# Kernel optimization log

Measured on AMD Instinct MI355X. Metric: run time of the kernel, lower is better.

Reference implementation:

```python
import jax, jax.numpy as jnp
import numpy as np

B, C, H, W = 4, 512, 56, 56
G, K = 16, 3
P = K * K
GC = C // G
DWK = 3
PAD = 1
OFFSET_SCALE = 1.0


def setup_inputs():
    key = jax.random.key(0)
    ks = jax.random.split(key, 10)

    def w(i, shape, sc=0.02):
        return jax.random.normal(ks[i], shape, jnp.float32) * sc

    return {
        "x": jax.random.normal(ks[0], (B, C, H, W), jnp.float32),
        "w_in": w(1, (C, C)), "b_in": jnp.zeros((C,), jnp.float32),
        "w_dw": w(2, (DWK, DWK, 1, C)), "b_dw": jnp.zeros((C,), jnp.float32),
        "ln_g": jnp.ones((C,), jnp.float32), "ln_b": jnp.zeros((C,), jnp.float32),
        "w_off": w(3, (C, G * P * 2)), "b_off": jnp.zeros((G * P * 2,), jnp.float32),
        "w_mask": w(4, (C, G * P)), "b_mask": jnp.zeros((G * P,), jnp.float32),
        "w_out": w(5, (C, C)), "b_out": jnp.zeros((C,), jnp.float32),
        "bn_g": jnp.ones((C,), jnp.float32), "bn_b": jnp.zeros((C,), jnp.float32),
        "bn_m": w(6, (C,), 0.1), "bn_v": jnp.abs(w(7, (C,), 0.1)) + 1.0,
    }


def _dcnv3_core(xp, offset, mask):
    """xp: [B,H,W,C]; offset: [B,H,W,G*P*2]; mask (softmaxed over P): [B,H,W,G,P]."""
    xpad = jnp.pad(xp, ((0, 0), (PAD, PAD), (PAD, PAD), (0, 0)))
    Hin, Win = H + 2 * PAD, W + 2 * PAD
    # normalized reference points (output-location centers in padded input coords)
    ref_x = (jnp.arange(W, dtype=jnp.float32) + 0.5 + (K - 1) // 2) / Win
    ref_y = (jnp.arange(H, dtype=jnp.float32) + 0.5 + (K - 1) // 2) / Hin
    # dilation grid, kx-major / ky-minor flattening (matches InternImage core)
    k = jnp.arange(K, dtype=jnp.float32) - (K - 1) // 2
    gx = jnp.repeat(k, K) / Win  # [P]
    gy = jnp.tile(k, K) / Hin    # [P]
    off = offset.reshape(B, H, W, G, P, 2)
    lx = ref_x[None, None, :, None, None] + gx * OFFSET_SCALE + off[..., 0] * OFFSET_SCALE / Win
    ly = ref_y[None, :, None, None, None] + gy * OFFSET_SCALE + off[..., 1] * OFFSET_SCALE / Hin
    # grid_sample semantics, align_corners=False, zero padding
    px = lx * Win - 0.5
    py = ly * Hin - 0.5
    x0f = jnp.floor(px)
    y0f = jnp.floor(py)
    tx = px - x0f
    ty = py - y0f
    x0 = x0f.astype(jnp.int32)
    y0 = y0f.astype(jnp.int32)
    flat = xpad.reshape(B, Hin * Win * G, GC)
    gidx = jnp.arange(G)[None, None, :, None]

    def corner(fb, yi, xi):
        valid = (yi >= 0) & (yi < Hin) & (xi >= 0) & (xi < Win)
        idx = (jnp.clip(yi, 0, Hin - 1) * Win + jnp.clip(xi, 0, Win - 1)) * G + gidx
        return jnp.take(fb, idx, axis=0) * valid[..., None]  # [H,W,G,P,GC]

    def sample_one(fb, y0b, x0b, tyb, txb):
        w00 = ((1 - tyb) * (1 - txb))[..., None]
        w01 = ((1 - tyb) * txb)[..., None]
        w10 = (tyb * (1 - txb))[..., None]
        w11 = (tyb * txb)[..., None]
        return (corner(fb, y0b, x0b) * w00 + corner(fb, y0b, x0b + 1) * w01
                + corner(fb, y0b + 1, x0b) * w10 + corner(fb, y0b + 1, x0b + 1) * w11)

    samp = jax.vmap(sample_one)(flat, y0, x0, ty, tx)  # [B,H,W,G,P,GC]
    return jnp.einsum('bhwgpc,bhwgp->bhwgc', samp, mask).reshape(B, H, W, C)


def reference(x, w_in, b_in, w_dw, b_dw, ln_g, ln_b, w_off, b_off, w_mask, b_mask, w_out, b_out, bn_g, bn_b, bn_m, bn_v):
    xh = jnp.transpose(x, (0, 2, 3, 1))  # NCHW -> NHWC
    xp = xh @ w_in + b_in                # input_proj
    # offset/mask branch: depthwise conv + LayerNorm(channels) + GELU
    x1 = jax.lax.conv_general_dilated(xh, w_dw, (1, 1), 'SAME', feature_group_count=C,
                                      dimension_numbers=('NHWC', 'HWIO', 'NHWC')) + b_dw
    mu = x1.mean(-1, keepdims=True)
    var = x1.var(-1, keepdims=True)
    x1 = (x1 - mu) / jnp.sqrt(var + 1e-6) * ln_g + ln_b
    x1 = jax.nn.gelu(x1, approximate=False)
    offset = x1 @ w_off + b_off
    mask = jax.nn.softmax((x1 @ w_mask + b_mask).reshape(B, H, W, G, P), axis=-1)
    y = _dcnv3_core(xp, offset, mask)
    y = y @ w_out + b_out                # output_proj
    y = jnp.transpose(y, (0, 3, 1, 2))   # NHWC -> NCHW
    # BatchNorm2d (inference: running stats) + SiLU
    y = (y - bn_m[:, None, None]) / jnp.sqrt(bn_v[:, None, None] + 1e-5) * bn_g[:, None, None] + bn_b[:, None, None]
    return jax.nn.silu(y)
```

## Files before the change

kernel.cpp:

```cpp
#include <hip/hip_runtime.h>
#include <cmath>

constexpr int B_ = 4, C_ = 512, H_ = 56, W_ = 56;
constexpr int HW_ = H_ * W_;
constexpr int NPIX = B_ * HW_;
constexpr int G_ = 16, P_ = 9;
constexpr int NMSK = G_ * P_;

typedef __attribute__((ext_vector_type(8))) short short8;
typedef __attribute__((ext_vector_type(4))) float f32x4;

__device__ __forceinline__ float b2f(ushort u) {
    union { unsigned int i; float f; } v; v.i = (unsigned int)u << 16; return v.f;
}
__device__ __forceinline__ ushort f2b(float f) {
    unsigned int x = __float_as_uint(f);
    unsigned int r = (x + 0x7fffu + ((x >> 16) & 1u)) >> 16;
    return (ushort)r;
}
__device__ __forceinline__ void gload16(const ushort* g, ushort* l) {
    __builtin_amdgcn_global_load_lds(
        (const __attribute__((address_space(1))) unsigned int*)g,
        (__attribute__((address_space(3))) unsigned int*)l, 16, 0, 0);
}

__global__ __launch_bounds__(256) void prep_weights_kernel(
    const float* __restrict__ w_in, const float* __restrict__ w_off,
    const float* __restrict__ w_mask, const float* __restrict__ w_out,
    const float* __restrict__ b_off, const float* __restrict__ b_mask,
    ushort* __restrict__ wtA, ushort* __restrict__ wtOM, ushort* __restrict__ wtO,
    float* __restrict__ bOM)
{
    __shared__ float tile[32][33];
    int z = blockIdx.z;
    int k0 = blockIdx.x * 32;
    int n0 = blockIdx.y * 32;
    int tx = threadIdx.x, ty = threadIdx.y;
    for (int i = ty; i < 32; i += 8) {
        int k = k0 + i, n = n0 + tx;
        float v;
        if (z == 0) v = w_in[k * 512 + n];
        else if (z == 1) v = w_out[k * 512 + n];
        else v = (n < 288) ? w_off[k * 288 + n]
                           : (n < 432 ? w_mask[k * 144 + (n - 288)] : 0.f);
        tile[i][tx] = v;
    }
    __syncthreads();
    ushort* dst = (z == 0) ? wtA : (z == 1 ? wtO : wtOM);
    for (int i = ty; i < 32; i += 8)
        dst[(size_t)(n0 + i) * 512 + k0 + tx] = f2b(tile[tx][i]);
    if (z == 2 && blockIdx.x == 0 && blockIdx.y == 0) {
        int t = ty * 32 + tx;
        for (int tt = t; tt < 512; tt += 256)
            bOM[tt] = (tt < 288) ? b_off[tt] : (tt < 432 ? b_mask[tt - 288] : 0.f);
    }
}

__global__ __launch_bounds__(256) void transpose_in_kernel(
    const float* __restrict__ in, ushort* __restrict__ out)
{
    __shared__ float tile[32][33];
    int b = blockIdx.z;
    int hw0 = blockIdx.x * 32;
    int c0 = blockIdx.y * 32;
    int tx = threadIdx.x, ty = threadIdx.y;
    const float* ib = in + (size_t)b * C_ * HW_;
    #pragma unroll
    for (int i = ty; i < 32; i += 8)
        tile[i][tx] = ib[(size_t)(c0 + i) * HW_ + hw0 + tx];
    __syncthreads();
    ushort* ob = out + (size_t)b * HW_ * C_;
    #pragma unroll
    for (int i = ty; i < 32; i += 8)
        ob[(size_t)(hw0 + i) * C_ + c0 + tx] = f2b(tile[tx][i]);
}

template <int MODE>
__global__ __launch_bounds__(256) void mfma_gemm_kernel(
    const ushort* __restrict__ A, const ushort* __restrict__ Bt,
    const float* __restrict__ bias, void* __restrict__ Cout,
    const float* __restrict__ bng, const float* __restrict__ bnb,
    const float* __restrict__ bnm, const float* __restrict__ bnv)
{
    __shared__ ushort As[128 * 64];
    __shared__ ushort Bs[128 * 64];
    int tid = threadIdx.x;
    int lane = tid & 63, wid = tid >> 6;
    int row0 = blockIdx.x * 128, col0 = blockIdx.y * 128;
    int wm = wid >> 1, wn = wid & 1;

    f32x4 acc[4][4] = {};

    int lr = lane >> 3;
    int sc = (lane & 7) ^ lr;

    for (int k0 = 0; k0 < 512; k0 += 64) {
        if (k0) __syncthreads();
        #pragma unroll
        for (int i = 0; i < 4; i++) {
            int rb = (wid * 4 + i) * 8;
            gload16(A + (size_t)(row0 + rb + lr) * 512 + k0 + sc * 8, &As[rb * 64]);
            gload16(Bt + (size_t)(col0 + rb + lr) * 512 + k0 + sc * 8, &Bs[rb * 64]);
        }
        __syncthreads();
        #pragma unroll
        for (int ks = 0; ks < 2; ks++) {
            short8 af[4], bf[4];
            #pragma unroll
            for (int mi = 0; mi < 4; mi++) {
                int r = wm * 64 + mi * 16 + (lane & 15);
                int c = ((lane >> 4) + ks * 4) ^ (r & 7);
                af[mi] = *(const short8*)((const char*)As + r * 128 + c * 16);
            }
            #pragma unroll
            for (int ni = 0; ni < 4; ni++) {
                int r = wn * 64 + ni * 16 + (lane & 15);
                int c = ((lane >> 4) + ks * 4) ^ (r & 7);
                bf[ni] = *(const short8*)((const char*)Bs + r * 128 + c * 16);
            }
            #pragma unroll
            for (int mi = 0; mi < 4; mi++)
                #pragma unroll
                for (int ni = 0; ni < 4; ni++)
                    acc[mi][ni] = __builtin_amdgcn_mfma_f32_16x16x32_bf16(
                        af[mi], bf[ni], acc[mi][ni], 0, 0, 0);
        }
    }

    #pragma unroll
    for (int ni = 0; ni < 4; ni++) {
        int col = col0 + wn * 64 + ni * 16 + (lane & 15);
        float bv = bias[col];
        float bsc = 0.f, bsh = 0.f;
        if constexpr (MODE == 2) {
            float inv = rsqrtf(bnv[col] + 1e-5f);
            bsc = bng[col] * inv;
            bsh = bnb[col] - bnm[col] * bsc;
        }
        #pragma unroll
        for (int mi = 0; mi < 4; mi++) {
            int rowb = row0 + wm * 64 + mi * 16 + (lane >> 4) * 4;
            #pragma unroll
            for (int r = 0; r < 4; r++) {
                float val = acc[mi][ni][r] + bv;
                if constexpr (MODE == 0) {
                    ((float*)Cout)[(size_t)(rowb + r) * 512 + col] = val;
                } else if constexpr (MODE == 1) {
                    ((ushort*)Cout)[(size_t)(rowb + r) * 512 + col] = f2b(val);
                } else {
                    int nn = rowb + r;
                    int bb = nn / HW_, hww = nn - bb * HW_;
                    float t2 = val * bsc + bsh;
                    float s = t2 / (1.f + expf(-t2));
                    ((float*)Cout)[((size_t)bb * C_ + col) * HW_ + hww] = s;
                }
            }
        }
    }
}

__global__ __launch_bounds__(256) void dwln_kernel(
    const ushort* __restrict__ xh, const float* __restrict__ wdw,
    const float* __restrict__ bdw, const float* __restrict__ lng,
    const float* __restrict__ lnb, ushort* __restrict__ x1)
{
    int tid = threadIdx.x;
    int wid = tid >> 6, lane = tid & 63;
    int n = blockIdx.x * 4 + wid;
    int b = n / HW_, hw = n % HW_;
    int h = hw / W_, w = hw % W_;
    int c0 = lane * 8;
    const ushort* base = xh + (size_t)b * HW_ * C_ + c0;

    uint4 nb[9];
    #pragma unroll
    for (int ky = 0; ky < 3; ky++)
        #pragma unroll
        for (int kx = 0; kx < 3; kx++) {
            int hh = h + ky - 1, ww = w + kx - 1;
            bool ok = (hh >= 0) & (hh < H_) & (ww >= 0) & (ww < W_);
            nb[ky * 3 + kx] = ok ? *(const uint4*)(base + ((size_t)hh * W_ + ww) * C_)
                                 : make_uint4(0u, 0u, 0u, 0u);
        }

    float acc[8];
    {
        float4 b0 = *(const float4*)&bdw[c0];
        float4 b1 = *(const float4*)&bdw[c0 + 4];
        acc[0] = b0.x; acc[1] = b0.y; acc[2] = b0.z; acc[3] = b0.w;
        acc[4] = b1.x; acc[5] = b1.y; acc[6] = b1.z; acc[7] = b1.w;
    }
    #pragma unroll
    for (int p = 0; p < 9; p++) {
        float4 w0 = *(const float4*)&wdw[p * C_ + c0];
        float4 w1 = *(const float4*)&wdw[p * C_ + c0 + 4];
        float wv[8] = {w0.x, w0.y, w0.z, w0.w, w1.x, w1.y, w1.z, w1.w};
        unsigned int u[4] = {nb[p].x, nb[p].y, nb[p].z, nb[p].w};
        #pragma unroll
        for (int q = 0; q < 4; q++) {
            float lo = __uint_as_float(u[q] << 16);
            float hi = __uint_as_float(u[q] & 0xffff0000u);
            acc[2 * q]     += wv[2 * q]     * lo;
            acc[2 * q + 1] += wv[2 * q + 1] * hi;
        }
    }

    float s1 = 0.f, s2 = 0.f;
    #pragma unroll
    for (int q = 0; q < 8; q++) { s1 += acc[q]; s2 += acc[q] * acc[q]; }
    #pragma unroll
    for (int o = 32; o > 0; o >>= 1) {
        s1 += __shfl_xor(s1, o);
        s2 += __shfl_xor(s2, o);
    }
    float mean = s1 * (1.f / 512.f);
    float var = s2 * (1.f / 512.f) - mean * mean;
    float inv = rsqrtf(var + 1e-6f);

    float4 g0 = *(const float4*)&lng[c0];
    float4 g1 = *(const float4*)&lng[c0 + 4];
    float4 e0 = *(const float4*)&lnb[c0];
    float4 e1 = *(const float4*)&lnb[c0 + 4];
    float gv[8] = {g0.x, g0.y, g0.z, g0.w, g1.x, g1.y, g1.z, g1.w};
    float ev[8] = {e0.x, e0.y, e0.z, e0.w, e1.x, e1.y, e1.z, e1.w};
    unsigned int outw[4];
    #pragma unroll
    for (int q = 0; q < 4; q++) {
        float t0 = (acc[2 * q]     - mean) * inv * gv[2 * q]     + ev[2 * q];
        float t1 = (acc[2 * q + 1] - mean) * inv * gv[2 * q + 1] + ev[2 * q + 1];
        float ge0 = 0.5f * t0 * (1.f + erff(t0 * 0.70710678118654752f));
        float ge1 = 0.5f * t1 * (1.f + erff(t1 * 0.70710678118654752f));
        outw[q] = (unsigned int)f2b(ge0) | ((unsigned int)f2b(ge1) << 16);
    }
    *(uint4*)&x1[(size_t)n * C_ + c0] = make_uint4(outw[0], outw[1], outw[2], outw[3]);
}

__global__ __launch_bounds__(256) void dcn_sample_kernel(
    const ushort* __restrict__ xp, const float* __restrict__ om,
    ushort* __restrict__ y1)
{
    __shared__ float slog[NMSK];
    __shared__ float sw4[NMSK][4];
    __shared__ int   sa4[NMSK][4];
    int bid = blockIdx.x;
    int n = (bid & 7) * (NPIX / 8) + (bid >> 3);
    int b = n / HW_, hw = n % HW_;
    int h = hw / W_, w = hw % W_;
    int tid = threadIdx.x;
    const float* omp = om + (size_t)n * 512;

    if (tid < NMSK) slog[tid] = omp[288 + tid];
    __syncthreads();
    if (tid < G_) {
        float mx = -1e30f;
        #pragma unroll
        for (int p = 0; p < P_; p++) mx = fmaxf(mx, slog[tid * P_ + p]);
        float e[P_], s = 0.f;
        #pragma unroll
        for (int p = 0; p < P_; p++) { e[p] = expf(slog[tid * P_ + p] - mx); s += e[p]; }
        float invs = 1.f / s;
        #pragma unroll
        for (int p = 0; p < P_; p++) slog[tid * P_ + p] = e[p] * invs;
    }
    __syncthreads();
    if (tid < NMSK) {
        int g = tid / 9, p = tid - g * 9;
        float ox = omp[g * 18 + p * 2 + 0];
        float oy = omp[g * 18 + p * 2 + 1];
        float px = (float)(w + (p / 3)) + ox;
        float py = (float)(h + (p % 3)) + oy;
        float x0f = floorf(px), y0f = floorf(py);
        float tx = px - x0f, ty = py - y0f;
        int x0 = (int)x0f, y0 = (int)y0f;
        float m = slog[tid];
        float ww[4] = { (1.f - ty) * (1.f - tx) * m, (1.f - ty) * tx * m,
                        ty * (1.f - tx) * m,         ty * tx * m };
        #pragma unroll
        for (int i = 0; i < 4; i++) {
            int yy = y0 + (i >> 1), xx = x0 + (i & 1);
            bool valid = (yy >= 1 && yy <= H_ && xx >= 1 && xx <= W_);
            sa4[tid][i] = valid ? ((yy - 1) * W_ + (xx - 1)) * C_ : 0;
            sw4[tid][i] = valid ? ww[i] : 0.f;
        }
    }
    __syncthreads();

    const ushort* xpb = xp + (size_t)b * HW_ * C_;
    int c0 = tid * 2;
    int g = tid >> 4;

    int addr[P_][4];
    #pragma unroll
    for (int p = 0; p < P_; p++)
        #pragma unroll
        for (int i = 0; i < 4; i++)
            addr[p][i] = sa4[g * 9 + p][i] + c0;

    unsigned int v[P_][4];
    #pragma unroll
    for (int p = 0; p < P_; p++)
        #pragma unroll
        for (int i = 0; i < 4; i++)
            v[p][i] = *(const unsigned int*)(xpb + addr[p][i]);

    float ax = 0.f, ay = 0.f;
    #pragma unroll
    for (int p = 0; p < P_; p++)
        #pragma unroll
        for (int i = 0; i < 4; i++) {
            float wgt = sw4[g * 9 + p][i];
            float lo = __uint_as_float(v[p][i] << 16);
            float hi = __uint_as_float(v[p][i] & 0xffff0000u);
            ax += wgt * lo;
            ay += wgt * hi;
        }

    ushort2 o; o.x = f2b(ax); o.y = f2b(ay);
    *(ushort2*)&y1[(size_t)n * 512 + c0] = o;
}

extern "C" void kernel_launch(void* const* d_in, const int* in_sizes, int n_in,
                              void* d_out, int out_size, void* d_ws, size_t ws_size,
                              hipStream_t stream)
{
    const float* x      = (const float*)d_in[0];
    const float* w_in   = (const float*)d_in[1];
    const float* b_in   = (const float*)d_in[2];
    const float* w_dw   = (const float*)d_in[3];
    const float* b_dw   = (const float*)d_in[4];
    const float* ln_g   = (const float*)d_in[5];
    const float* ln_b   = (const float*)d_in[6];
    const float* w_off  = (const float*)d_in[7];
    const float* b_off  = (const float*)d_in[8];
    const float* w_mask = (const float*)d_in[9];
    const float* b_mask = (const float*)d_in[10];
    const float* w_out  = (const float*)d_in[11];
    const float* b_out  = (const float*)d_in[12];
    const float* bn_g   = (const float*)d_in[13];
    const float* bn_b   = (const float*)d_in[14];
    const float* bn_m   = (const float*)d_in[15];
    const float* bn_v   = (const float*)d_in[16];
    float* out = (float*)d_out;

    const size_t NC = (size_t)NPIX * C_;
    char* wsp = (char*)d_ws;
    ushort* xh  = (ushort*)wsp;  wsp += NC * 2;
    ushort* x1  = (ushort*)wsp;  wsp += NC * 2;
    ushort* xpb = (ushort*)wsp;  wsp += NC * 2;
    float*  om  = (float*)wsp;   wsp += NC * 4;
    ushort* wtA = (ushort*)wsp;  wsp += 512 * 512 * 2;
    ushort* wtOM= (ushort*)wsp;  wsp += 512 * 512 * 2;
    ushort* wtO = (ushort*)wsp;  wsp += 512 * 512 * 2;
    float*  bOM = (float*)wsp;   wsp += 512 * 4;

    dim3 tb(32, 8);
    prep_weights_kernel<<<dim3(16, 16, 3), tb, 0, stream>>>(
        w_in, w_off, w_mask, w_out, b_off, b_mask, wtA, wtOM, wtO, bOM);

    transpose_in_kernel<<<dim3(HW_ / 32, C_ / 32, B_), tb, 0, stream>>>(x, xh);

    mfma_gemm_kernel<1><<<dim3(NPIX / 128, 4), 256, 0, stream>>>(
        xh, wtA, b_in, xpb, nullptr, nullptr, nullptr, nullptr);

    dwln_kernel<<<NPIX / 4, 256, 0, stream>>>(xh, w_dw, b_dw, ln_g, ln_b, x1);

    mfma_gemm_kernel<0><<<dim3(NPIX / 128, 4), 256, 0, stream>>>(
        x1, wtOM, bOM, om, nullptr, nullptr, nullptr, nullptr);

    dcn_sample_kernel<<<NPIX, 256, 0, stream>>>(xpb, om, x1 );

    mfma_gemm_kernel<2><<<dim3(NPIX / 128, 4), 256, 0, stream>>>(
        x1, wtO, b_out, out, bn_g, bn_b, bn_m, bn_v);
}
```

Baseline: 129.2 us.

## Split BN+SiLU into transposing kernel and remap GEMM block order across XCDs

The output GEMM previously wrote NCHW directly with a strided scatter, so adjacent lanes stored to addresses far apart. It now writes row-major fp32 into the om buffer, and a separate tiled-transpose kernel applies BatchNorm and SiLU with coalesced NCHW stores. All GEMMs also move to a 1D grid of 392 blocks, remapped so consecutive block IDs (round-robined across 8 XCDs) land on nearby tiles for better L2 locality. The cost is an extra launch plus an fp32 intermediate write and read of the full output.

New measurement: 126.5 us. 2.1% less time.

```diff
diff --git a/kernel.cpp b/kernel.cpp
--- a/kernel.cpp
+++ b/kernel.cpp
@@ -78,15 +78,15 @@
 template <int MODE>
 __global__ __launch_bounds__(256) void mfma_gemm_kernel(
     const ushort* __restrict__ A, const ushort* __restrict__ Bt,
-    const float* __restrict__ bias, void* __restrict__ Cout,
-    const float* __restrict__ bng, const float* __restrict__ bnb,
-    const float* __restrict__ bnm, const float* __restrict__ bnv)
+    const float* __restrict__ bias, void* __restrict__ Cout)
 {
     __shared__ ushort As[128 * 64];
     __shared__ ushort Bs[128 * 64];
     int tid = threadIdx.x;
     int lane = tid & 63, wid = tid >> 6;
-    int row0 = blockIdx.x * 128, col0 = blockIdx.y * 128;
+    int bid = blockIdx.x;
+    int wgid = (bid & 7) * 49 + (bid >> 3);
+    int row0 = (wgid >> 2) * 128, col0 = (wgid & 3) * 128;
     int wm = wid >> 1, wn = wid & 1;
 
     f32x4 acc[4][4] = {};
@@ -131,29 +131,16 @@
     for (int ni = 0; ni < 4; ni++) {
         int col = col0 + wn * 64 + ni * 16 + (lane & 15);
         float bv = bias[col];
-        float bsc = 0.f, bsh = 0.f;
-        if constexpr (MODE == 2) {
-            float inv = rsqrtf(bnv[col] + 1e-5f);
-            bsc = bng[col] * inv;
-            bsh = bnb[col] - bnm[col] * bsc;
-        }
         #pragma unroll
         for (int mi = 0; mi < 4; mi++) {
             int rowb = row0 + wm * 64 + mi * 16 + (lane >> 4) * 4;
             #pragma unroll
             for (int r = 0; r < 4; r++) {
                 float val = acc[mi][ni][r] + bv;
-                if constexpr (MODE == 0) {
+                if constexpr (MODE == 0)
                     ((float*)Cout)[(size_t)(rowb + r) * 512 + col] = val;
-                } else if constexpr (MODE == 1) {
+                else
                     ((ushort*)Cout)[(size_t)(rowb + r) * 512 + col] = f2b(val);
-                } else {
-                    int nn = rowb + r;
-                    int bb = nn / HW_, hww = nn - bb * HW_;
-                    float t2 = val * bsc + bsh;
-                    float s = t2 / (1.f + expf(-t2));
-                    ((float*)Cout)[((size_t)bb * C_ + col) * HW_ + hww] = s;
-                }
             }
         }
     }
@@ -317,6 +304,33 @@
 
     ushort2 o; o.x = f2b(ax); o.y = f2b(ay);
     *(ushort2*)&y1[(size_t)n * 512 + c0] = o;
+}
+
+__global__ __launch_bounds__(256) void bn_out_kernel(
+    const float* __restrict__ in, float* __restrict__ out,
+    const float* __restrict__ bng, const float* __restrict__ bnb,
+    const float* __restrict__ bnm, const float* __restrict__ bnv)
+{
+    __shared__ float tile[32][33];
+    int b = blockIdx.z;
+    int hw0 = blockIdx.x * 32;
+    int c0 = blockIdx.y * 32;
+    int tx = threadIdx.x, ty = threadIdx.y;
+    const float* ib = in + (size_t)b * HW_ * C_;
+    #pragma unroll
+    for (int i = ty; i < 32; i += 8)
+        tile[i][tx] = ib[(size_t)(hw0 + i) * C_ + c0 + tx];
+    __syncthreads();
+    float* ob = out + (size_t)b * C_ * HW_;
+    #pragma unroll
+    for (int i = ty; i < 32; i += 8) {
+        int c = c0 + i;
+        float t = tile[tx][i];
+        float inv = rsqrtf(bnv[c] + 1e-5f);
+        float t2 = (t - bnm[c]) * inv * bng[c] + bnb[c];
+        float s = t2 / (1.f + expf(-t2));
+        ob[(size_t)c * HW_ + hw0 + tx] = s;
+    }
 }
 
 extern "C" void kernel_launch(void* const* d_in, const int* in_sizes, int n_in,
@@ -359,16 +373,16 @@
 
     transpose_in_kernel<<<dim3(HW_ / 32, C_ / 32, B_), tb, 0, stream>>>(x, xh);
 
-    mfma_gemm_kernel<1><<<dim3(NPIX / 128, 4), 256, 0, stream>>>(
-        xh, wtA, b_in, xpb, nullptr, nullptr, nullptr, nullptr);
+    mfma_gemm_kernel<1><<<392, 256, 0, stream>>>(xh, wtA, b_in, xpb);
 
     dwln_kernel<<<NPIX / 4, 256, 0, stream>>>(xh, w_dw, b_dw, ln_g, ln_b, x1);
 
-    mfma_gemm_kernel<0><<<dim3(NPIX / 128, 4), 256, 0, stream>>>(
-        x1, wtOM, bOM, om, nullptr, nullptr, nullptr, nullptr);
+    mfma_gemm_kernel<0><<<392, 256, 0, stream>>>(x1, wtOM, bOM, om);
 
     dcn_sample_kernel<<<NPIX, 256, 0, stream>>>(xpb, om, x1 );
 
-    mfma_gemm_kernel<2><<<dim3(NPIX / 128, 4), 256, 0, stream>>>(
-        x1, wtO, b_out, out, bn_g, bn_b, bn_m, bn_v);
-}
+    mfma_gemm_kernel<0><<<392, 256, 0, stream>>>(x1, wtO, b_out, om);
+
+    bn_out_kernel<<<dim3(HW_ / 32, C_ / 32, B_), tb, 0, stream>>>(
+        om, out, bn_g, bn_b, bn_m, bn_v);
+}
```
